# Optimization experiments

Measured on AMD Instinct MI355X. Metric: run time of the kernel, lower is better.

The kernel has to match this reference:

```python
import jax, jax.numpy as jnp
import numpy as np

NU, NV, D, H, E = 100000, 50000, 128, 128, 1600000
ALPHA = 0.2  # LeakyReLU slope


def _spmm(rows, cols, vals, x, n_rows):
    # sparse [n_rows, n_cols] @ dense [n_cols, d] via gather + segment_sum
    return jax.ops.segment_sum(vals[:, None] * x[cols], rows, num_segments=n_rows)


def _gcn(x, rows, cols, vals, n_rows, W, b):
    support = x @ W + b  # bias added before spmm is equivalent only if... original adds after spmm
    return None


def _gcn_layer(x, rows, cols, vals, n_rows, W, b):
    support = x @ W
    out = _spmm(rows, cols, vals, support, n_rows) + b
    return jnp.where(out >= 0, out, ALPHA * out)  # LeakyReLU


def _reparam(mean, logstd, noise):
    sigma = jnp.exp(0.1 + 0.9 * jax.nn.softplus(logstd))
    return noise * sigma + mean


def setup_inputs() -> dict:
    key = jax.random.key(0)
    ks = jax.random.split(key, 24)
    stdv = 1.0 / np.sqrt(H)
    u = lambda k, shp, s: jax.random.uniform(k, shp, jnp.float32, -s, s)
    inp = {
        "ufea": jax.random.normal(ks[0], (NU, D), jnp.float32),
        "vfea": jax.random.normal(ks[1], (NV, D), jnp.float32),
        "uv_rows": jax.random.randint(ks[2], (E,), 0, NU, jnp.int32),
        "uv_cols": jax.random.randint(ks[3], (E,), 0, NV, jnp.int32),
        "uv_vals": jax.random.uniform(ks[4], (E,), jnp.float32),
        "vu_rows": jax.random.randint(ks[5], (E,), 0, NV, jnp.int32),
        "vu_cols": jax.random.randint(ks[6], (E,), 0, NU, jnp.int32),
        "vu_vals": jax.random.uniform(ks[7], (E,), jnp.float32),
        "noise_u": jax.random.normal(ks[8], (NU, H), jnp.float32),
        "noise_v": jax.random.normal(ks[9], (NV, H), jnp.float32),
        "gc1_W": u(ks[10], (D, H), stdv), "gc1_b": u(ks[11], (H,), stdv),
        "gc3m_W": u(ks[12], (H, H), stdv), "gc3m_b": u(ks[13], (H,), stdv),
        "gc3s_W": u(ks[14], (H, H), stdv), "gc3s_b": u(ks[15], (H,), stdv),
        "um_W": u(ks[16], (2 * H, H), stdv), "um_b": u(ks[17], (H,), stdv),
        "us_W": u(ks[18], (2 * H, H), stdv), "us_b": u(ks[19], (H,), stdv),
        "im_W": u(ks[20], (2 * H, H), stdv), "im_b": u(ks[21], (H,), stdv),
        "is_W": u(ks[22], (2 * H, H), stdv), "is_b": u(ks[23], (H,), stdv),
    }
    return inp


def reference(ufea, vfea, uv_rows, uv_cols, uv_vals, vu_rows, vu_cols, vu_vals,
              noise_u, noise_v, gc1_W, gc1_b, gc3m_W, gc3m_b, gc3s_W, gc3s_b,
              um_W, um_b, us_W, us_b, im_W, im_b, is_W, is_b):
    nu, nv = ufea.shape[0], vfea.shape[0]
    # user path: VU_adj [nv, nu] then UV_adj [nu, nv]
    user_ho = _gcn_layer(ufea, vu_rows, vu_cols, vu_vals, nv, gc1_W, gc1_b)        # [nv, H]
    user_ho_mean = _gcn_layer(user_ho, uv_rows, uv_cols, uv_vals, nu, gc3m_W, gc3m_b)  # [nu, H]
    user_ho_logstd = _gcn_layer(user_ho, uv_rows, uv_cols, uv_vals, nu, gc3s_W, gc3s_b)
    user_mean = jnp.concatenate((user_ho_mean, ufea), axis=1) @ um_W + um_b
    user_logstd = jnp.concatenate((user_ho_logstd, ufea), axis=1) @ us_W + us_b
    user_z = _reparam(user_mean, user_logstd, noise_u)
    # item path: UV_adj [nu, nv] then VU_adj [nv, nu]
    item_ho = _gcn_layer(vfea, uv_rows, uv_cols, uv_vals, nu, gc1_W, gc1_b)        # [nu, H]
    item_ho_mean = _gcn_layer(item_ho, vu_rows, vu_cols, vu_vals, nv, gc3m_W, gc3m_b)  # [nv, H]
    item_ho_logstd = _gcn_layer(item_ho, vu_rows, vu_cols, vu_vals, nv, gc3s_W, gc3s_b)
    item_mean = jnp.concatenate((item_ho_mean, vfea), axis=1) @ im_W + im_b
    item_logstd = jnp.concatenate((item_ho_logstd, vfea), axis=1) @ is_W + is_b
    item_z = _reparam(item_mean, item_logstd, noise_v)
    return user_z, item_z
```

## Files before the change

kernel.cpp:

```cpp
#include <hip/hip_runtime.h>
#include <math.h>

typedef float f32x4 __attribute__((ext_vector_type(4)));
typedef __bf16 bf16x8 __attribute__((ext_vector_type(8)));

#define LRELU_ALPHA 0.2f

__global__ void edge_count(const int* __restrict__ rows, int* __restrict__ cnt, int E) {
    int i = blockIdx.x * 256 + threadIdx.x;
    if (i < E) atomicAdd(&cnt[rows[i]], 1);
}

__global__ __launch_bounds__(512) void scan1(const int* __restrict__ in, int* __restrict__ out,
                                             int* __restrict__ bsum, int ncnt, int nout) {
    __shared__ int s[512];
    int t = threadIdx.x;
    int i = blockIdx.x * 512 + t;
    int v = (i < ncnt) ? in[i] : 0;
    s[t] = v; __syncthreads();
    for (int o = 1; o < 512; o <<= 1) {
        int u = (t >= o) ? s[t - o] : 0;
        __syncthreads();
        s[t] += u;
        __syncthreads();
    }
    if (i < nout) out[i] = s[t] - v;
    if (t == 511) bsum[blockIdx.x] = s[511];
}

__global__ void scan2(int* __restrict__ b, int nb) {
    __shared__ int s[256];
    int t = threadIdx.x;
    int v = (t < nb) ? b[t] : 0;
    s[t] = v; __syncthreads();
    for (int o = 1; o < 256; o <<= 1) {
        int u = (t >= o) ? s[t - o] : 0;
        __syncthreads();
        s[t] += u;
        __syncthreads();
    }
    if (t < nb) b[t] = s[t] - v;
}

__global__ __launch_bounds__(512) void scan3(int* __restrict__ out, const int* __restrict__ bsum, int nout) {
    int i = blockIdx.x * 512 + threadIdx.x;
    if (i < nout) out[i] += bsum[blockIdx.x];
}

__global__ void edge_fill(const int* __restrict__ rows, const int* __restrict__ cols,
                          const float* __restrict__ vals, int* __restrict__ cur,
                          int* __restrict__ ocol, float* __restrict__ oval, int E) {
    int i = blockIdx.x * 256 + threadIdx.x;
    if (i < E) {
        int r = rows[i];
        int p = atomicAdd(&cur[r], 1);
        ocol[p] = cols[i];
        oval[p] = vals[i];
    }
}

__global__ void prep_frag(const float* __restrict__ W, unsigned short* __restrict__ Fh,
                          unsigned short* __restrict__ Fl, int K) {
    int o = blockIdx.x * 256 + threadIdx.x;
    if (o >= K * 128) return;
    int j = o & 7;
    int lane = (o >> 3) & 63;
    int blk = o >> 9;
    int nc = blk & 7, kh = blk >> 3;
    int col = nc * 16 + (lane & 15);
    int k = kh * 32 + (lane >> 4) * 8 + j;
    float f = W[k * 128 + col];
    __bf16 h = (__bf16)f;
    __bf16 l = (__bf16)(f - (float)h);
    Fh[o] = __builtin_bit_cast(unsigned short, h);
    Fl[o] = __builtin_bit_cast(unsigned short, l);
}

__global__ __launch_bounds__(256) void spmm_lrelu(const int* __restrict__ ptr, const int* __restrict__ cols,
                                                  const float* __restrict__ vals, const float* __restrict__ x,
                                                  const float* __restrict__ bias, float* __restrict__ out,
                                                  int nrows) {
    int w = (blockIdx.x << 2) + (threadIdx.x >> 6);
    if (w >= nrows) return;
    int lane = threadIdx.x & 63;
    int s = ptr[w], e = ptr[w + 1];
    const float2* __restrict__ x2 = (const float2*)x;
    float ax = 0.f, ay = 0.f;
    int i = s;
    for (; i + 3 < e; i += 4) {
        int c0 = cols[i], c1 = cols[i + 1], c2 = cols[i + 2], c3 = cols[i + 3];
        float v0 = vals[i], v1 = vals[i + 1], v2 = vals[i + 2], v3 = vals[i + 3];
        float2 g0 = x2[(size_t)c0 * 64 + lane];
        float2 g1 = x2[(size_t)c1 * 64 + lane];
        float2 g2 = x2[(size_t)c2 * 64 + lane];
        float2 g3 = x2[(size_t)c3 * 64 + lane];
        ax += v0 * g0.x + v1 * g1.x + v2 * g2.x + v3 * g3.x;
        ay += v0 * g0.y + v1 * g1.y + v2 * g2.y + v3 * g3.y;
    }
    for (; i < e; i++) {
        int c = cols[i]; float v = vals[i];
        float2 g = x2[(size_t)c * 64 + lane];
        ax += v * g.x; ay += v * g.y;
    }
    float2 b2 = ((const float2*)bias)[lane];
    ax += b2.x; ay += b2.y;
    ax = ax >= 0.f ? ax : LRELU_ALPHA * ax;
    ay = ay >= 0.f ? ay : LRELU_ALPHA * ay;
    float2 o; o.x = ax; o.y = ay;
    ((float2*)out)[(size_t)w * 64 + lane] = o;
}

template <int KPH, int EPI>
__global__ __launch_bounds__(256) void gemm_reg(const float* __restrict__ A1, const float* __restrict__ A2,
                                                const unsigned short* __restrict__ Fh,
                                                const unsigned short* __restrict__ Fl,
                                                const float* __restrict__ bias,
                                                const float* __restrict__ noise,
                                                float* __restrict__ C, int M) {
    const int t = threadIdx.x;
    const int lane = t & 63;
    const int w = t >> 6;
    const int l15 = lane & 15, l4 = lane >> 4;
    const int row0 = blockIdx.x * 128 + w * 32;

    f32x4 acc[2][8] = {};

#pragma unroll
    for (int kh = 0; kh < KPH; kh++) {
        const float* Asrc;
        int kk;
        if constexpr (KPH == 8) {
            Asrc = (kh < 4) ? A1 : A2;
            kk = (kh & 3) * 32 + l4 * 8;
        } else {
            Asrc = A1;
            kk = kh * 32 + l4 * 8;
        }
        bf16x8 ah[2], al[2];
#pragma unroll
        for (int mr = 0; mr < 2; mr++) {
            int r = row0 + mr * 16 + l15;
            float4 f0, f1;
            if (r < M) {
                const float* p = Asrc + (size_t)r * 128 + kk;
                f0 = *(const float4*)p;
                f1 = *(const float4*)(p + 4);
            } else {
                f0 = make_float4(0.f, 0.f, 0.f, 0.f);
                f1 = f0;
            }
            float fv[8] = {f0.x, f0.y, f0.z, f0.w, f1.x, f1.y, f1.z, f1.w};
#pragma unroll
            for (int j = 0; j < 8; j++) {
                __bf16 h = (__bf16)fv[j];
                ah[mr][j] = h;
                al[mr][j] = (__bf16)(fv[j] - (float)h);
            }
        }
        const unsigned short* bh_base = Fh + (size_t)kh * 4096;
        const unsigned short* bl_base = Fl + (size_t)kh * 4096;
#pragma unroll
        for (int nc = 0; nc < 8; nc++) {
            bf16x8 bh = *(const bf16x8*)(bh_base + nc * 512 + lane * 8);
            bf16x8 bl = *(const bf16x8*)(bl_base + nc * 512 + lane * 8);
#pragma unroll
            for (int mr = 0; mr < 2; mr++) {
                acc[mr][nc] = __builtin_amdgcn_mfma_f32_16x16x32_bf16(ah[mr], bh, acc[mr][nc], 0, 0, 0);
                acc[mr][nc] = __builtin_amdgcn_mfma_f32_16x16x32_bf16(ah[mr], bl, acc[mr][nc], 0, 0, 0);
                acc[mr][nc] = __builtin_amdgcn_mfma_f32_16x16x32_bf16(al[mr], bh, acc[mr][nc], 0, 0, 0);
            }
        }
    }

#pragma unroll
    for (int mr = 0; mr < 2; mr++) {
        int rowb = row0 + mr * 16 + l4 * 4;
#pragma unroll
        for (int nc = 0; nc < 8; nc++) {
            int col = nc * 16 + l15;
#pragma unroll
            for (int j = 0; j < 4; j++) {
                int r = rowb + j;
                if (r < M) {
                    float v = acc[mr][nc][j];
                    if constexpr (EPI == 0) {
                        C[(size_t)r * 128 + col] = v;
                    } else if constexpr (EPI == 1) {
                        C[(size_t)r * 128 + col] = v + bias[col];
                    } else {
                        float mean = v + bias[col];
                        float ls = C[(size_t)r * 128 + col];
                        float sp = ls > 0.f ? ls + log1pf(expf(-ls)) : log1pf(expf(ls));
                        float sg = expf(0.1f + 0.9f * sp);
                        C[(size_t)r * 128 + col] = noise[(size_t)r * 128 + col] * sg + mean;
                    }
                }
            }
        }
    }
}

extern "C" void kernel_launch(void* const* d_in, const int* in_sizes, int n_in,
                              void* d_out, int out_size, void* d_ws, size_t ws_size,
                              hipStream_t stream) {
    const float* ufea    = (const float*)d_in[0];
    const float* vfea    = (const float*)d_in[1];
    const int*   uv_rows = (const int*)d_in[2];
    const int*   uv_cols = (const int*)d_in[3];
    const float* uv_vals = (const float*)d_in[4];
    const int*   vu_rows = (const int*)d_in[5];
    const int*   vu_cols = (const int*)d_in[6];
    const float* vu_vals = (const float*)d_in[7];
    const float* noise_u = (const float*)d_in[8];
    const float* noise_v = (const float*)d_in[9];
    const float* gc1_W  = (const float*)d_in[10];
    const float* gc1_b  = (const float*)d_in[11];
    const float* gc3m_W = (const float*)d_in[12];
    const float* gc3m_b = (const float*)d_in[13];
    const float* gc3s_W = (const float*)d_in[14];
    const float* gc3s_b = (const float*)d_in[15];
    const float* um_W = (const float*)d_in[16];
    const float* um_b = (const float*)d_in[17];
    const float* us_W = (const float*)d_in[18];
    const float* us_b = (const float*)d_in[19];
    const float* im_W = (const float*)d_in[20];
    const float* im_b = (const float*)d_in[21];
    const float* is_W = (const float*)d_in[22];
    const float* is_b = (const float*)d_in[23];

    const int H  = in_sizes[11];
    const int D  = in_sizes[10] / H;
    const int NU = in_sizes[0] / D;
    const int NV = in_sizes[1] / D;
    const int E  = in_sizes[2];

    char* ws = (char*)d_ws;
    size_t off = 0;
    auto alloc = [&](size_t bytes) -> char* {
        char* p = ws + off;
        off = (off + bytes + 255) & ~(size_t)255;
        return p;
    };
    unsigned short* wf_gc1_h  = (unsigned short*)alloc(128 * 128 * 2);
    unsigned short* wf_gc1_l  = (unsigned short*)alloc(128 * 128 * 2);
    unsigned short* wf_gc3m_h = (unsigned short*)alloc(128 * 128 * 2);
    unsigned short* wf_gc3m_l = (unsigned short*)alloc(128 * 128 * 2);
    unsigned short* wf_gc3s_h = (unsigned short*)alloc(128 * 128 * 2);
    unsigned short* wf_gc3s_l = (unsigned short*)alloc(128 * 128 * 2);
    unsigned short* wf_um_h = (unsigned short*)alloc(256 * 128 * 2);
    unsigned short* wf_um_l = (unsigned short*)alloc(256 * 128 * 2);
    unsigned short* wf_us_h = (unsigned short*)alloc(256 * 128 * 2);
    unsigned short* wf_us_l = (unsigned short*)alloc(256 * 128 * 2);
    unsigned short* wf_im_h = (unsigned short*)alloc(256 * 128 * 2);
    unsigned short* wf_im_l = (unsigned short*)alloc(256 * 128 * 2);
    unsigned short* wf_is_h = (unsigned short*)alloc(256 * 128 * 2);
    unsigned short* wf_is_l = (unsigned short*)alloc(256 * 128 * 2);
    int*   ptr_uv = (int*)alloc((size_t)(NU + 1) * 4);
    int*   cur_uv = (int*)alloc((size_t)NU * 4);
    int*   col_uv = (int*)alloc((size_t)E * 4);
    float* val_uv = (float*)alloc((size_t)E * 4);
    int*   ptr_vu = (int*)alloc((size_t)(NV + 1) * 4);
    int*   cur_vu = (int*)alloc((size_t)NV * 4);
    int*   col_vu = (int*)alloc((size_t)E * 4);
    float* val_vu = (float*)alloc((size_t)E * 4);
    int*   bsum   = (int*)alloc(1024 * 4);
    float* bufA = (float*)alloc((size_t)NU * 128 * 4);
    float* bufB = (float*)alloc((size_t)NU * 128 * 4);

    float* outU = (float*)d_out;
    float* outI = outU + (size_t)NU * H;

    const int eb = (E + 255) / 256;
    const int nbU = (NU + 1 + 511) / 512;
    const int nbV = (NV + 1 + 511) / 512;
    const int gU = (NU + 127) / 128, gV = (NV + 127) / 128;
    const int sU = (NU + 3) / 4, sV = (NV + 3) / 4;

    hipMemsetAsync(cur_uv, 0, (size_t)NU * 4, stream);
    hipMemsetAsync(cur_vu, 0, (size_t)NV * 4, stream);
    edge_count<<<eb, 256, 0, stream>>>(uv_rows, cur_uv, E);
    edge_count<<<eb, 256, 0, stream>>>(vu_rows, cur_vu, E);
    scan1<<<nbU, 512, 0, stream>>>(cur_uv, ptr_uv, bsum, NU, NU + 1);
    scan2<<<1, 256, 0, stream>>>(bsum, nbU);
    scan3<<<nbU, 512, 0, stream>>>(ptr_uv, bsum, NU + 1);
    scan1<<<nbV, 512, 0, stream>>>(cur_vu, ptr_vu, bsum, NV, NV + 1);
    scan2<<<1, 256, 0, stream>>>(bsum, nbV);
    scan3<<<nbV, 512, 0, stream>>>(ptr_vu, bsum, NV + 1);
    hipMemcpyAsync(cur_uv, ptr_uv, (size_t)NU * 4, hipMemcpyDeviceToDevice, stream);
    hipMemcpyAsync(cur_vu, ptr_vu, (size_t)NV * 4, hipMemcpyDeviceToDevice, stream);
    edge_fill<<<eb, 256, 0, stream>>>(uv_rows, uv_cols, uv_vals, cur_uv, col_uv, val_uv, E);
    edge_fill<<<eb, 256, 0, stream>>>(vu_rows, vu_cols, vu_vals, cur_vu, col_vu, val_vu, E);

    prep_frag<<<64, 256, 0, stream>>>(gc1_W, wf_gc1_h, wf_gc1_l, 128);
    prep_frag<<<64, 256, 0, stream>>>(gc3m_W, wf_gc3m_h, wf_gc3m_l, 128);
    prep_frag<<<64, 256, 0, stream>>>(gc3s_W, wf_gc3s_h, wf_gc3s_l, 128);
    prep_frag<<<128, 256, 0, stream>>>(um_W, wf_um_h, wf_um_l, 256);
    prep_frag<<<128, 256, 0, stream>>>(us_W, wf_us_h, wf_us_l, 256);
    prep_frag<<<128, 256, 0, stream>>>(im_W, wf_im_h, wf_im_l, 256);
    prep_frag<<<128, 256, 0, stream>>>(is_W, wf_is_h, wf_is_l, 256);

    gemm_reg<4, 0><<<gU, 256, 0, stream>>>(ufea, nullptr, wf_gc1_h, wf_gc1_l, nullptr, nullptr, bufA, NU);
    spmm_lrelu<<<sV, 256, 0, stream>>>(ptr_vu, col_vu, val_vu, bufA, gc1_b, bufB, NV);
    gemm_reg<4, 0><<<gV, 256, 0, stream>>>(bufB, nullptr, wf_gc3s_h, wf_gc3s_l, nullptr, nullptr, bufA, NV);
    spmm_lrelu<<<sU, 256, 0, stream>>>(ptr_uv, col_uv, val_uv, bufA, gc3s_b, outU, NU);
    gemm_reg<8, 1><<<gU, 256, 0, stream>>>(outU, ufea, wf_us_h, wf_us_l, us_b, nullptr, outU, NU);
    gemm_reg<4, 0><<<gV, 256, 0, stream>>>(bufB, nullptr, wf_gc3m_h, wf_gc3m_l, nullptr, nullptr, bufA, NV);
    spmm_lrelu<<<sU, 256, 0, stream>>>(ptr_uv, col_uv, val_uv, bufA, gc3m_b, bufB, NU);
    gemm_reg<8, 2><<<gU, 256, 0, stream>>>(bufB, ufea, wf_um_h, wf_um_l, um_b, noise_u, outU, NU);

    gemm_reg<4, 0><<<gV, 256, 0, stream>>>(vfea, nullptr, wf_gc1_h, wf_gc1_l, nullptr, nullptr, bufA, NV);
    spmm_lrelu<<<sU, 256, 0, stream>>>(ptr_uv, col_uv, val_uv, bufA, gc1_b, bufB, NU);
    gemm_reg<4, 0><<<gU, 256, 0, stream>>>(bufB, nullptr, wf_gc3s_h, wf_gc3s_l, nullptr, nullptr, bufA, NU);
    spmm_lrelu<<<sV, 256, 0, stream>>>(ptr_vu, col_vu, val_vu, bufA, gc3s_b, outI, NV);
    gemm_reg<8, 1><<<gV, 256, 0, stream>>>(outI, vfea, wf_is_h, wf_is_l, is_b, nullptr, outI, NV);
    gemm_reg<4, 0><<<gU, 256, 0, stream>>>(bufB, nullptr, wf_gc3m_h, wf_gc3m_l, nullptr, nullptr, bufA, NU);
    spmm_lrelu<<<sV, 256, 0, stream>>>(ptr_vu, col_vu, val_vu, bufA, gc3m_b, bufB, NV);
    gemm_reg<8, 2><<<gV, 256, 0, stream>>>(bufB, vfea, wf_im_h, wf_im_l, im_b, noise_v, outI, NV);

    (void)n_in; (void)out_size; (void)ws_size;
}
```

Measured before the change: 1.832 ms.

## Fuse mean/logstd GCN branches and store intermediates as split-bf16 pairs

The mean and logstd GCN layers now share one GEMM, one SpMM and one final GEMM, each handling both weight sets. The softplus/reparam epilogue is fused into the last GEMM, so the separate logstd pass and its extra round trip are gone. Intermediates are stored as packed bf16 hi/lo pairs in the layout the MFMA fragments need, which removes the per-tile fp32-to-bf16 split in later GEMMs. GEMM tiles drop to 64 rows per block and use an LDS transpose for coalesced stores, which adds register and LDS pressure.

```diff
diff --git a/kernel.cpp b/kernel.cpp
--- a/kernel.cpp
+++ b/kernel.cpp
@@ -5,6 +5,21 @@
 typedef __bf16 bf16x8 __attribute__((ext_vector_type(8)));
 
 #define LRELU_ALPHA 0.2f
+
+static __device__ __forceinline__ unsigned short f2b(float f) {
+    __bf16 h = (__bf16)f;
+    return __builtin_bit_cast(unsigned short, h);
+}
+static __device__ __forceinline__ float b2f(unsigned short s) {
+    unsigned int u = ((unsigned int)s) << 16;
+    return __builtin_bit_cast(float, u);
+}
+static __device__ __forceinline__ void dsplit(float f, unsigned short& h, unsigned short& l) {
+    h = f2b(f);
+    l = f2b(f - b2f(h));
+}
+static __device__ __forceinline__ float ulo(unsigned int u) { return __builtin_bit_cast(float, u << 16); }
+static __device__ __forceinline__ float uhi(unsigned int u) { return __builtin_bit_cast(float, u & 0xFFFF0000u); }
 
 __global__ void edge_count(const int* __restrict__ rows, int* __restrict__ cnt, int E) {
     int i = blockIdx.x * 256 + threadIdx.x;
@@ -69,131 +84,236 @@
     int nc = blk & 7, kh = blk >> 3;
     int col = nc * 16 + (lane & 15);
     int k = kh * 32 + (lane >> 4) * 8 + j;
-    float f = W[k * 128 + col];
-    __bf16 h = (__bf16)f;
-    __bf16 l = (__bf16)(f - (float)h);
-    Fh[o] = __builtin_bit_cast(unsigned short, h);
-    Fl[o] = __builtin_bit_cast(unsigned short, l);
-}
-
-__global__ __launch_bounds__(256) void spmm_lrelu(const int* __restrict__ ptr, const int* __restrict__ cols,
-                                                  const float* __restrict__ vals, const float* __restrict__ x,
-                                                  const float* __restrict__ bias, float* __restrict__ out,
-                                                  int nrows) {
+    unsigned short h, l;
+    dsplit(W[k * 128 + col], h, l);
+    Fh[o] = h; Fl[o] = l;
+}
+
+__global__ __launch_bounds__(256) void spmm1(const int* __restrict__ ptr, const int* __restrict__ cols,
+                                             const float* __restrict__ vals, const char* __restrict__ xb,
+                                             const float* __restrict__ bias, char* __restrict__ ob, int nrows) {
     int w = (blockIdx.x << 2) + (threadIdx.x >> 6);
     if (w >= nrows) return;
     int lane = threadIdx.x & 63;
+    int loff = lane * 8;
     int s = ptr[w], e = ptr[w + 1];
-    const float2* __restrict__ x2 = (const float2*)x;
     float ax = 0.f, ay = 0.f;
     int i = s;
     for (; i + 3 < e; i += 4) {
         int c0 = cols[i], c1 = cols[i + 1], c2 = cols[i + 2], c3 = cols[i + 3];
         float v0 = vals[i], v1 = vals[i + 1], v2 = vals[i + 2], v3 = vals[i + 3];
-        float2 g0 = x2[(size_t)c0 * 64 + lane];
-        float2 g1 = x2[(size_t)c1 * 64 + lane];
-        float2 g2 = x2[(size_t)c2 * 64 + lane];
-        float2 g3 = x2[(size_t)c3 * 64 + lane];
-        ax += v0 * g0.x + v1 * g1.x + v2 * g2.x + v3 * g3.x;
-        ay += v0 * g0.y + v1 * g1.y + v2 * g2.y + v3 * g3.y;
+        uint2 u0 = *(const uint2*)(xb + (size_t)c0 * 512 + loff);
+        uint2 u1 = *(const uint2*)(xb + (size_t)c1 * 512 + loff);
+        uint2 u2 = *(const uint2*)(xb + (size_t)c2 * 512 + loff);
+        uint2 u3 = *(const uint2*)(xb + (size_t)c3 * 512 + loff);
+        ax += v0 * (ulo(u0.x) + ulo(u0.y)) + v1 * (ulo(u1.x) + ulo(u1.y))
+            + v2 * (ulo(u2.x) + ulo(u2.y)) + v3 * (ulo(u3.x) + ulo(u3.y));
+        ay += v0 * (uhi(u0.x) + uhi(u0.y)) + v1 * (uhi(u1.x) + uhi(u1.y))
+            + v2 * (uhi(u2.x) + uhi(u2.y)) + v3 * (uhi(u3.x) + uhi(u3.y));
     }
     for (; i < e; i++) {
         int c = cols[i]; float v = vals[i];
-        float2 g = x2[(size_t)c * 64 + lane];
-        ax += v * g.x; ay += v * g.y;
+        uint2 u = *(const uint2*)(xb + (size_t)c * 512 + loff);
+        ax += v * (ulo(u.x) + ulo(u.y));
+        ay += v * (uhi(u.x) + uhi(u.y));
     }
     float2 b2 = ((const float2*)bias)[lane];
     ax += b2.x; ay += b2.y;
     ax = ax >= 0.f ? ax : LRELU_ALPHA * ax;
     ay = ay >= 0.f ? ay : LRELU_ALPHA * ay;
-    float2 o; o.x = ax; o.y = ay;
-    ((float2*)out)[(size_t)w * 64 + lane] = o;
-}
-
-template <int KPH, int EPI>
-__global__ __launch_bounds__(256) void gemm_reg(const float* __restrict__ A1, const float* __restrict__ A2,
-                                                const unsigned short* __restrict__ Fh,
-                                                const unsigned short* __restrict__ Fl,
-                                                const float* __restrict__ bias,
-                                                const float* __restrict__ noise,
-                                                float* __restrict__ C, int M) {
+    unsigned short h0, l0, h1, l1;
+    dsplit(ax, h0, l0); dsplit(ay, h1, l1);
+    *(uint2*)(ob + (size_t)w * 512 + loff) =
+        make_uint2((unsigned)h0 | ((unsigned)h1 << 16), (unsigned)l0 | ((unsigned)l1 << 16));
+}
+
+__global__ __launch_bounds__(256) void spmm2(const int* __restrict__ ptr, const int* __restrict__ cols,
+                                             const float* __restrict__ vals, const char* __restrict__ xb,
+                                             const float* __restrict__ bm, const float* __restrict__ bs,
+                                             char* __restrict__ ob, int nrows) {
+    int w = (blockIdx.x << 2) + (threadIdx.x >> 6);
+    if (w >= nrows) return;
+    int lane = threadIdx.x & 63;
+    int loff = lane * 8;
+    int s = ptr[w], e = ptr[w + 1];
+    float mx = 0.f, my = 0.f, sx = 0.f, sy = 0.f;
+    int i = s;
+    for (; i + 1 < e; i += 2) {
+        int c0 = cols[i], c1 = cols[i + 1];
+        float v0 = vals[i], v1 = vals[i + 1];
+        const char* p0 = xb + (size_t)c0 * 1024 + loff;
+        const char* p1 = xb + (size_t)c1 * 1024 + loff;
+        uint2 m0 = *(const uint2*)p0, s0 = *(const uint2*)(p0 + 512);
+        uint2 m1 = *(const uint2*)p1, s1 = *(const uint2*)(p1 + 512);
+        mx += v0 * (ulo(m0.x) + ulo(m0.y)) + v1 * (ulo(m1.x) + ulo(m1.y));
+        my += v0 * (uhi(m0.x) + uhi(m0.y)) + v1 * (uhi(m1.x) + uhi(m1.y));
+        sx += v0 * (ulo(s0.x) + ulo(s0.y)) + v1 * (ulo(s1.x) + ulo(s1.y));
+        sy += v0 * (uhi(s0.x) + uhi(s0.y)) + v1 * (uhi(s1.x) + uhi(s1.y));
+    }
+    for (; i < e; i++) {
+        int c = cols[i]; float v = vals[i];
+        const char* p = xb + (size_t)c * 1024 + loff;
+        uint2 m0 = *(const uint2*)p, s0 = *(const uint2*)(p + 512);
+        mx += v * (ulo(m0.x) + ulo(m0.y));
+        my += v * (uhi(m0.x) + uhi(m0.y));
+        sx += v * (ulo(s0.x) + ulo(s0.y));
+        sy += v * (uhi(s0.x) + uhi(s0.y));
+    }
+    float2 bm2 = ((const float2*)bm)[lane];
+    float2 bs2 = ((const float2*)bs)[lane];
+    mx += bm2.x; my += bm2.y; sx += bs2.x; sy += bs2.y;
+    mx = mx >= 0.f ? mx : LRELU_ALPHA * mx;
+    my = my >= 0.f ? my : LRELU_ALPHA * my;
+    sx = sx >= 0.f ? sx : LRELU_ALPHA * sx;
+    sy = sy >= 0.f ? sy : LRELU_ALPHA * sy;
+    unsigned short h0, l0, h1, l1;
+    char* po = ob + (size_t)w * 1024 + loff;
+    dsplit(mx, h0, l0); dsplit(my, h1, l1);
+    *(uint2*)po = make_uint2((unsigned)h0 | ((unsigned)h1 << 16), (unsigned)l0 | ((unsigned)l1 << 16));
+    dsplit(sx, h0, l0); dsplit(sy, h1, l1);
+    *(uint2*)(po + 512) = make_uint2((unsigned)h0 | ((unsigned)h1 << 16), (unsigned)l0 | ((unsigned)l1 << 16));
+}
+
+static __device__ __forceinline__ void load32(const char* p, bf16x8& h8, bf16x8& l8) {
+    uint4 u0 = *(const uint4*)p;
+    uint4 u1 = *(const uint4*)(p + 16);
+    union { unsigned int u[4]; bf16x8 v; } H, L;
+    H.u[0] = u0.x; H.u[1] = u0.z; H.u[2] = u1.x; H.u[3] = u1.z;
+    L.u[0] = u0.y; L.u[1] = u0.w; L.u[2] = u1.y; L.u[3] = u1.w;
+    h8 = H.v; l8 = L.v;
+}
+static __device__ __forceinline__ void split8(float4 f0, float4 f1, bf16x8& h8, bf16x8& l8) {
+    float fv[8] = {f0.x, f0.y, f0.z, f0.w, f1.x, f1.y, f1.z, f1.w};
+#pragma unroll
+    for (int j = 0; j < 8; j++) {
+        __bf16 h = (__bf16)fv[j];
+        h8[j] = h;
+        l8[j] = (__bf16)(fv[j] - (float)h);
+    }
+}
+static __device__ __forceinline__ f32x4 acc3(f32x4 a, bf16x8 xh, bf16x8 xl, bf16x8 bh, bf16x8 bl) {
+    a = __builtin_amdgcn_mfma_f32_16x16x32_bf16(xh, bh, a, 0, 0, 0);
+    a = __builtin_amdgcn_mfma_f32_16x16x32_bf16(xh, bl, a, 0, 0, 0);
+    a = __builtin_amdgcn_mfma_f32_16x16x32_bf16(xl, bh, a, 0, 0, 0);
+    return a;
+}
+
+template <int MODE>
+__global__ __launch_bounds__(256) void gemm_u(const char* __restrict__ A1, const float* __restrict__ A2f,
+                                              const unsigned short* __restrict__ F1h, const unsigned short* __restrict__ F1l,
+                                              const unsigned short* __restrict__ F2h, const unsigned short* __restrict__ F2l,
+                                              const float* __restrict__ bias1, const float* __restrict__ bias2,
+                                              const float* __restrict__ noise, float* __restrict__ out,
+                                              char* __restrict__ outb, int M) {
+    __shared__ float xpose[4][2080];
     const int t = threadIdx.x;
     const int lane = t & 63;
     const int w = t >> 6;
     const int l15 = lane & 15, l4 = lane >> 4;
-    const int row0 = blockIdx.x * 128 + w * 32;
-
-    f32x4 acc[2][8] = {};
-
+    const int rowW = blockIdx.x * 64 + w * 16;
+    int ar = rowW + l15;
+    const int arc = (ar < M) ? ar : (M - 1);
+    float* lds = xpose[w];
+
+    f32x4 accM[8] = {};
+    f32x4 accS[8] = {};
+
+    constexpr int KPH = (MODE == 2) ? 8 : 4;
 #pragma unroll
     for (int kh = 0; kh < KPH; kh++) {
-        const float* Asrc;
-        int kk;
-        if constexpr (KPH == 8) {
-            Asrc = (kh < 4) ? A1 : A2;
-            kk = (kh & 3) * 32 + l4 * 8;
+        const int kk = (kh & 3) * 32 + l4 * 8;
+        bf16x8 amh, aml, xsh, xsl;
+        if constexpr (MODE == 0) {
+            const float* p = A2f + (size_t)arc * 128 + kk;
+            split8(*(const float4*)p, *(const float4*)(p + 4), amh, aml);
+            xsh = amh; xsl = aml;
+        } else if constexpr (MODE == 1) {
+            load32(A1 + (size_t)arc * 512 + (size_t)kk * 4, amh, aml);
+            xsh = amh; xsl = aml;
         } else {
-            Asrc = A1;
-            kk = kh * 32 + l4 * 8;
-        }
-        bf16x8 ah[2], al[2];
-#pragma unroll
-        for (int mr = 0; mr < 2; mr++) {
-            int r = row0 + mr * 16 + l15;
-            float4 f0, f1;
+            if (kh < 4) {
+                load32(A1 + (size_t)arc * 1024 + (size_t)kk * 4, amh, aml);
+                load32(A1 + (size_t)arc * 1024 + 512 + (size_t)kk * 4, xsh, xsl);
+            } else {
+                const float* p = A2f + (size_t)arc * 128 + kk;
+                split8(*(const float4*)p, *(const float4*)(p + 4), amh, aml);
+                xsh = amh; xsl = aml;
+            }
+        }
+        const unsigned short* f1h = F1h + (size_t)kh * 4096;
+        const unsigned short* f1l = F1l + (size_t)kh * 4096;
+        const unsigned short* f2h = F2h + (size_t)kh * 4096;
+        const unsigned short* f2l = F2l + (size_t)kh * 4096;
+#pragma unroll
+        for (int nc = 0; nc < 8; nc++) {
+            bf16x8 b1h = *(const bf16x8*)(f1h + nc * 512 + lane * 8);
+            bf16x8 b1l = *(const bf16x8*)(f1l + nc * 512 + lane * 8);
+            accM[nc] = acc3(accM[nc], amh, aml, b1h, b1l);
+            if constexpr (MODE >= 1) {
+                bf16x8 b2h = *(const bf16x8*)(f2h + nc * 512 + lane * 8);
+                bf16x8 b2l = *(const bf16x8*)(f2l + nc * 512 + lane * 8);
+                accS[nc] = acc3(accS[nc], xsh, xsl, b2h, b2l);
+            }
+        }
+    }
+
+    if constexpr (MODE == 2) {
+#pragma unroll
+        for (int nc = 0; nc < 8; nc++) {
+            int c = nc * 16 + l15;
+            float b1 = bias1[c], b2v = bias2[c];
+#pragma unroll
+            for (int j = 0; j < 4; j++) {
+                int r = rowW + l4 * 4 + j;
+                int rc = (r < M) ? r : (M - 1);
+                float mean = accM[nc][j] + b1;
+                float ls = accS[nc][j] + b2v;
+                float sp = ls > 0.f ? ls + log1pf(expf(-ls)) : log1pf(expf(ls));
+                float sg = expf(0.1f + 0.9f * sp);
+                lds[(l4 * 4 + j) * 130 + c] = noise[(size_t)rc * 128 + c] * sg + mean;
+            }
+        }
+#pragma unroll
+        for (int p = 0; p < 16; p++) {
+            int r = rowW + p;
             if (r < M) {
-                const float* p = Asrc + (size_t)r * 128 + kk;
-                f0 = *(const float4*)p;
-                f1 = *(const float4*)(p + 4);
-            } else {
-                f0 = make_float4(0.f, 0.f, 0.f, 0.f);
-                f1 = f0;
-            }
-            float fv[8] = {f0.x, f0.y, f0.z, f0.w, f1.x, f1.y, f1.z, f1.w};
-#pragma unroll
-            for (int j = 0; j < 8; j++) {
-                __bf16 h = (__bf16)fv[j];
-                ah[mr][j] = h;
-                al[mr][j] = (__bf16)(fv[j] - (float)h);
-            }
-        }
-        const unsigned short* bh_base = Fh + (size_t)kh * 4096;
-        const unsigned short* bl_base = Fl + (size_t)kh * 4096;
-#pragma unroll
-        for (int nc = 0; nc < 8; nc++) {
-            bf16x8 bh = *(const bf16x8*)(bh_base + nc * 512 + lane * 8);
-            bf16x8 bl = *(const bf16x8*)(bl_base + nc * 512 + lane * 8);
-#pragma unroll
-            for (int mr = 0; mr < 2; mr++) {
-                acc[mr][nc] = __builtin_amdgcn_mfma_f32_16x16x32_bf16(ah[mr], bh, acc[mr][nc], 0, 0, 0);
-                acc[mr][nc] = __builtin_amdgcn_mfma_f32_16x16x32_bf16(ah[mr], bl, acc[mr][nc], 0, 0, 0);
-                acc[mr][nc] = __builtin_amdgcn_mfma_f32_16x16x32_bf16(al[mr], bh, acc[mr][nc], 0, 0, 0);
-            }
-        }
-    }
-
-#pragma unroll
-    for (int mr = 0; mr < 2; mr++) {
-        int rowb = row0 + mr * 16 + l4 * 4;
-#pragma unroll
-        for (int nc = 0; nc < 8; nc++) {
-            int col = nc * 16 + l15;
-#pragma unroll
-            for (int j = 0; j < 4; j++) {
-                int r = rowb + j;
+                float2 f = *(const float2*)&lds[p * 130 + lane * 2];
+                *(float2*)(out + (size_t)r * 128 + lane * 2) = f;
+            }
+        }
+    } else {
+        const size_t rstride = (MODE == 0) ? 512 : 1024;
+#pragma unroll
+        for (int nc = 0; nc < 8; nc++)
+#pragma unroll
+            for (int j = 0; j < 4; j++)
+                lds[(l4 * 4 + j) * 130 + nc * 16 + l15] = accM[nc][j];
+#pragma unroll
+        for (int p = 0; p < 16; p++) {
+            int r = rowW + p;
+            if (r < M) {
+                float2 f = *(const float2*)&lds[p * 130 + lane * 2];
+                unsigned short h0, l0, h1, l1;
+                dsplit(f.x, h0, l0); dsplit(f.y, h1, l1);
+                *(uint2*)(outb + (size_t)r * rstride + lane * 8) =
+                    make_uint2((unsigned)h0 | ((unsigned)h1 << 16), (unsigned)l0 | ((unsigned)l1 << 16));
+            }
+        }
+        if constexpr (MODE == 1) {
+#pragma unroll
+            for (int nc = 0; nc < 8; nc++)
+#pragma unroll
+                for (int j = 0; j < 4; j++)
+                    lds[(l4 * 4 + j) * 130 + nc * 16 + l15] = accS[nc][j];
+#pragma unroll
+            for (int p = 0; p < 16; p++) {
+                int r = rowW + p;
                 if (r < M) {
-                    float v = acc[mr][nc][j];
-                    if constexpr (EPI == 0) {
-                        C[(size_t)r * 128 + col] = v;
-                    } else if constexpr (EPI == 1) {
-                        C[(size_t)r * 128 + col] = v + bias[col];
-                    } else {
-                        float mean = v + bias[col];
-                        float ls = C[(size_t)r * 128 + col];
-                        float sp = ls > 0.f ? ls + log1pf(expf(-ls)) : log1pf(expf(ls));
-                        float sg = expf(0.1f + 0.9f * sp);
-                        C[(size_t)r * 128 + col] = noise[(size_t)r * 128 + col] * sg + mean;
-                    }
+                    float2 f = *(const float2*)&lds[p * 130 + lane * 2];
+                    unsigned short h0, l0, h1, l1;
+                    dsplit(f.x, h0, l0); dsplit(f.y, h1, l1);
+                    *(uint2*)(outb + (size_t)r * rstride + 512 + lane * 8) =
+                        make_uint2((unsigned)h0 | ((unsigned)h1 << 16), (unsigned)l0 | ((unsigned)l1 << 16));
                 }
             }
         }
@@ -241,20 +361,20 @@
         off = (off + bytes + 255) & ~(size_t)255;
         return p;
     };
-    unsigned short* wf_gc1_h  = (unsigned short*)alloc(128 * 128 * 2);
-    unsigned short* wf_gc1_l  = (unsigned short*)alloc(128 * 128 * 2);
-    unsigned short* wf_gc3m_h = (unsigned short*)alloc(128 * 128 * 2);
-    unsigned short* wf_gc3m_l = (unsigned short*)alloc(128 * 128 * 2);
-    unsigned short* wf_gc3s_h = (unsigned short*)alloc(128 * 128 * 2);
-    unsigned short* wf_gc3s_l = (unsigned short*)alloc(128 * 128 * 2);
-    unsigned short* wf_um_h = (unsigned short*)alloc(256 * 128 * 2);
-    unsigned short* wf_um_l = (unsigned short*)alloc(256 * 128 * 2);
-    unsigned short* wf_us_h = (unsigned short*)alloc(256 * 128 * 2);
-    unsigned short* wf_us_l = (unsigned short*)alloc(256 * 128 * 2);
-    unsigned short* wf_im_h = (unsigned short*)alloc(256 * 128 * 2);
-    unsigned short* wf_im_l = (unsigned short*)alloc(256 * 128 * 2);
-    unsigned short* wf_is_h = (unsigned short*)alloc(256 * 128 * 2);
-    unsigned short* wf_is_l = (unsigned short*)alloc(256 * 128 * 2);
+    unsigned short* f_gc1_h  = (unsigned short*)alloc(128 * 128 * 2);
+    unsigned short* f_gc1_l  = (unsigned short*)alloc(128 * 128 * 2);
+    unsigned short* f_gc3m_h = (unsigned short*)alloc(128 * 128 * 2);
+    unsigned short* f_gc3m_l = (unsigned short*)alloc(128 * 128 * 2);
+    unsigned short* f_gc3s_h = (unsigned short*)alloc(128 * 128 * 2);
+    unsigned short* f_gc3s_l = (unsigned short*)alloc(128 * 128 * 2);
+    unsigned short* f_um_h = (unsigned short*)alloc(256 * 128 * 2);
+    unsigned short* f_um_l = (unsigned short*)alloc(256 * 128 * 2);
+    unsigned short* f_us_h = (unsigned short*)alloc(256 * 128 * 2);
+    unsigned short* f_us_l = (unsigned short*)alloc(256 * 128 * 2);
+    unsigned short* f_im_h = (unsigned short*)alloc(256 * 128 * 2);
+    unsigned short* f_im_l = (unsigned short*)alloc(256 * 128 * 2);
+    unsigned short* f_is_h = (unsigned short*)alloc(256 * 128 * 2);
+    unsigned short* f_is_l = (unsigned short*)alloc(256 * 128 * 2);
     int*   ptr_uv = (int*)alloc((size_t)(NU + 1) * 4);
     int*   cur_uv = (int*)alloc((size_t)NU * 4);
     int*   col_uv = (int*)alloc((size_t)E * 4);
@@ -264,8 +384,9 @@
     int*   col_vu = (int*)alloc((size_t)E * 4);
     float* val_vu = (float*)alloc((size_t)E * 4);
     int*   bsum   = (int*)alloc(1024 * 4);
-    float* bufA = (float*)alloc((size_t)NU * 128 * 4);
-    float* bufB = (float*)alloc((size_t)NU * 128 * 4);
+    char* P = alloc((size_t)NU * 1024);
+    char* Q = alloc((size_t)NU * 512);
+    char* R = alloc((size_t)NV * 512);
 
     float* outU = (float*)d_out;
     float* outI = outU + (size_t)NU * H;
@@ -273,7 +394,7 @@
     const int eb = (E + 255) / 256;
     const int nbU = (NU + 1 + 511) / 512;
     const int nbV = (NV + 1 + 511) / 512;
-    const int gU = (NU + 127) / 128, gV = (NV + 127) / 128;
+    const int gU = (NU + 63) / 64, gV = (NV + 63) / 64;
     const int sU = (NU + 3) / 4, sV = (NV + 3) / 4;
 
     hipMemsetAsync(cur_uv, 0, (size_t)NU * 4, stream);
@@ -291,31 +412,31 @@
     edge_fill<<<eb, 256, 0, stream>>>(uv_rows, uv_cols, uv_vals, cur_uv, col_uv, val_uv, E);
     edge_fill<<<eb, 256, 0, stream>>>(vu_rows, vu_cols, vu_vals, cur_vu, col_vu, val_vu, E);
 
-    prep_frag<<<64, 256, 0, stream>>>(gc1_W, wf_gc1_h, wf_gc1_l, 128);
-    prep_frag<<<64, 256, 0, stream>>>(gc3m_W, wf_gc3m_h, wf_gc3m_l, 128);
-    prep_frag<<<64, 256, 0, stream>>>(gc3s_W, wf_gc3s_h, wf_gc3s_l, 128);
-    prep_frag<<<128, 256, 0, stream>>>(um_W, wf_um_h, wf_um_l, 256);
-    prep_frag<<<128, 256, 0, stream>>>(us_W, wf_us_h, wf_us_l, 256);
-    prep_frag<<<128, 256, 0, stream>>>(im_W, wf_im_h, wf_im_l, 256);
-    prep_frag<<<128, 256, 0, stream>>>(is_W, wf_is_h, wf_is_l, 256);
-
-    gemm_reg<4, 0><<<gU, 256, 0, stream>>>(ufea, nullptr, wf_gc1_h, wf_gc1_l, nullptr, nullptr, bufA, NU);
-    spmm_lrelu<<<sV, 256, 0, stream>>>(ptr_vu, col_vu, val_vu, bufA, gc1_b, bufB, NV);
-    gemm_reg<4, 0><<<gV, 256, 0, stream>>>(bufB, nullptr, wf_gc3s_h, wf_gc3s_l, nullptr, nullptr, bufA, NV);
-    spmm_lrelu<<<sU, 256, 0, stream>>>(ptr_uv, col_uv, val_uv, bufA, gc3s_b, outU, NU);
-    gemm_reg<8, 1><<<gU, 256, 0, stream>>>(outU, ufea, wf_us_h, wf_us_l, us_b, nullptr, outU, NU);
-    gemm_reg<4, 0><<<gV, 256, 0, stream>>>(bufB, nullptr, wf_gc3m_h, wf_gc3m_l, nullptr, nullptr, bufA, NV);
-    spmm_lrelu<<<sU, 256, 0, stream>>>(ptr_uv, col_uv, val_uv, bufA, gc3m_b, bufB, NU);
-    gemm_reg<8, 2><<<gU, 256, 0, stream>>>(bufB, ufea, wf_um_h, wf_um_l, um_b, noise_u, outU, NU);
-
-    gemm_reg<4, 0><<<gV, 256, 0, stream>>>(vfea, nullptr, wf_gc1_h, wf_gc1_l, nullptr, nullptr, bufA, NV);
-    spmm_lrelu<<<sU, 256, 0, stream>>>(ptr_uv, col_uv, val_uv, bufA, gc1_b, bufB, NU);
-    gemm_reg<4, 0><<<gU, 256, 0, stream>>>(bufB, nullptr, wf_gc3s_h, wf_gc3s_l, nullptr, nullptr, bufA, NU);
-    spmm_lrelu<<<sV, 256, 0, stream>>>(ptr_vu, col_vu, val_vu, bufA, gc3s_b, outI, NV);
-    gemm_reg<8, 1><<<gV, 256, 0, stream>>>(outI, vfea, wf_is_h, wf_is_l, is_b, nullptr, outI, NV);
-    gemm_reg<4, 0><<<gU, 256, 0, stream>>>(bufB, nullptr, wf_gc3m_h, wf_gc3m_l, nullptr, nullptr, bufA, NU);
-    spmm_lrelu<<<sV, 256, 0, stream>>>(ptr_vu, col_vu, val_vu, bufA, gc3m_b, bufB, NV);
-    gemm_reg<8, 2><<<gV, 256, 0, stream>>>(bufB, vfea, wf_im_h, wf_im_l, im_b, noise_v, outI, NV);
+    prep_frag<<<64, 256, 0, stream>>>(gc1_W, f_gc1_h, f_gc1_l, 128);
+    prep_frag<<<64, 256, 0, stream>>>(gc3m_W, f_gc3m_h, f_gc3m_l, 128);
+    prep_frag<<<64, 256, 0, stream>>>(gc3s_W, f_gc3s_h, f_gc3s_l, 128);
+    prep_frag<<<128, 256, 0, stream>>>(um_W, f_um_h, f_um_l, 256);
+    prep_frag<<<128, 256, 0, stream>>>(us_W, f_us_h, f_us_l, 256);
+    prep_frag<<<128, 256, 0, stream>>>(im_W, f_im_h, f_im_l, 256);
+    prep_frag<<<128, 256, 0, stream>>>(is_W, f_is_h, f_is_l, 256);
+
+    gemm_u<0><<<gU, 256, 0, stream>>>(nullptr, ufea, f_gc1_h, f_gc1_l, nullptr, nullptr,
+                                      nullptr, nullptr, nullptr, nullptr, Q, NU);
+    spmm1<<<sV, 256, 0, stream>>>(ptr_vu, col_vu, val_vu, Q, gc1_b, R, NV);
+    gemm_u<1><<<gV, 256, 0, stream>>>(R, nullptr, f_gc3m_h, f_gc3m_l, f_gc3s_h, f_gc3s_l,
+                                      nullptr, nullptr, nullptr, nullptr, Q, NV);
+    spmm2<<<sU, 256, 0, stream>>>(ptr_uv, col_uv, val_uv, Q, gc3m_b, gc3s_b, P, NU);
+    gemm_u<2><<<gU, 256, 0, stream>>>(P, ufea, f_um_h, f_um_l, f_us_h, f_us_l,
+                                      um_b, us_b, noise_u, outU, nullptr, NU);
+
+    gemm_u<0><<<gV, 256, 0, stream>>>(nullptr, vfea, f_gc1_h, f_gc1_l, nullptr, nullptr,
+                                      nullptr, nullptr, nullptr, nullptr, R, NV);
+    spmm1<<<sU, 256, 0, stream>>>(ptr_uv, col_uv, val_uv, R, gc1_b, Q, NU);
+    gemm_u<1><<<gU, 256, 0, stream>>>(Q, nullptr, f_gc3m_h, f_gc3m_l, f_gc3s_h, f_gc3s_l,
+                                      nullptr, nullptr, nullptr, nullptr, P, NU);
+    spmm2<<<sV, 256, 0, stream>>>(ptr_vu, col_vu, val_vu, P, gc3m_b, gc3s_b, Q, NV);
+    gemm_u<2><<<gV, 256, 0, stream>>>(Q, vfea, f_im_h, f_im_l, f_is_h, f_is_l,
+                                      im_b, is_b, noise_v, outI, nullptr, NV);
 
     (void)n_in; (void)out_size; (void)ws_size;
 }
```

New measurement: 1.837 ms. Within noise of the previous version (+0.3%).
